# Optimization experiments

Measured on AMD Instinct MI355X. Metric: run time of the kernel, lower is better.

Reference implementation:

```python
import jax, jax.numpy as jnp
import numpy as np
from jax import lax

# Geometry derived from calc_block_params_and_padding_1d(32, 1024, 3, 1):
N, H, W, C = 1, 1024, 1024, 64
CO, K = 64, 3
BC = 32        # blocks per spatial dim (bcount)
BS = 34        # input block size (bsize)
BSO = 32       # output block size (bsize_out)
BSTR = 32      # block stride (bstride)
PAD = 1        # pad=2 total -> 1 top/left, 1 bottom/right
M = 512
EPS = 1e-3     # bn_eps


def setup_inputs() -> dict:
    key = jax.random.key(0)
    ks = jax.random.split(key, 8)
    inp_NHWC = jax.random.normal(ks[0], (N, H, W, C), jnp.float32)
    conv_w = jax.random.normal(ks[1], (K, K, C, CO), jnp.float32) * 0.05  # HWIO
    conv_b = jax.random.normal(ks[2], (CO,), jnp.float32) * 0.1
    gamma = 1.0 + 0.1 * jax.random.normal(ks[3], (CO,), jnp.float32)
    beta = 0.1 * jax.random.normal(ks[4], (CO,), jnp.float32)
    running_mean = 0.1 * jax.random.normal(ks[5], (CO,), jnp.float32)
    running_var = jax.random.uniform(ks[6], (CO,), jnp.float32, 0.5, 1.5)
    # active blocks: random subset of the 32x32 block grid, sorted flat ids
    flat = jnp.sort(jax.random.permutation(ks[7], BC * BC)[:M]).astype(jnp.int32)
    active_block_indices = jnp.stack(
        [jnp.zeros((M,), jnp.int32), flat // BC, flat % BC], axis=1)  # (n, i, j)
    return dict(inp_NHWC=inp_NHWC, conv_w=conv_w, conv_b=conv_b, gamma=gamma,
                beta=beta, running_mean=running_mean, running_var=running_var,
                active_block_indices=active_block_indices)


def reference(inp_NHWC, conv_w, conv_b, gamma, beta, running_mean, running_var,
              active_block_indices):
    # pad (as torch F.pad(0,0,1,1,1,1) on NHWC): pad H and W by 1 each side
    x = jnp.pad(inp_NHWC, ((0, 0), (PAD, PAD), (PAD, PAD), (0, 0)))
    n = active_block_indices[:, 0]
    i = active_block_indices[:, 1]
    j = active_block_indices[:, 2]

    # sparse_gather: extract [M, BS, BS, C] active tiles
    def gather(nn, ii, jj):
        return lax.dynamic_slice(x, (nn, ii * BSTR, jj * BSTR, 0), (1, BS, BS, C))[0]
    p = jax.vmap(gather)(n, i, j)  # [M, 34, 34, C]

    # conv (VALID, stride 1) + inference BatchNorm + ReLU
    q = lax.conv_general_dilated(p, conv_w, (1, 1), 'VALID',
                                 dimension_numbers=('NHWC', 'HWIO', 'NHWC'))
    q = q + conv_b
    scale = gamma * lax.rsqrt(running_var + EPS)
    q = jnp.maximum(q * scale + (beta - running_mean * scale), 0.0)  # [M, 32, 32, CO]

    # sparse_scatter (add=False): blocks tile the output exactly (BSO == BSTR)
    out6 = jnp.zeros((N, BC, BSO, BC, BSO, CO), inp_NHWC.dtype)
    out6 = out6.at[n, i, :, j].set(q)  # advanced idx -> [M, BSO, BSO, CO]
    return out6.reshape(N, BC * BSO, BC * BSO, CO)
```

## Files before the change

kernel.cpp:

```cpp
#include <hip/hip_runtime.h>

typedef _Float16 f16;
typedef f16 f16x8 __attribute__((ext_vector_type(8)));
typedef float f32x4 __attribute__((ext_vector_type(4)));

#define IMG_H 1024
#define IMG_W 1024
#define CIN 64
#define COUT_ 64
#define NBLK 32
#define NACT 512
#define EPS_ 1e-3f

#define WT_ELEMS (18 * 4 * 64 * 8)
#define WT_BYTES (WT_ELEMS * 2)
#define FLAGS_OFF WT_BYTES

__global__ void prep_weights_k(const float* __restrict__ w, f16* __restrict__ wt) {
    int t = blockIdx.x * 256 + threadIdx.x;
    if (t >= WT_ELEMS) return;
    int j  = t & 7;
    int l  = (t >> 3) & 63;
    int wv = (t >> 9) & 3;
    int kk = t >> 11;
    int ky = kk / 6;
    int kx = (kk % 6) >> 1;
    int hf = kk & 1;
    int cin  = hf * 32 + ((l >> 4) << 3) + j;
    int cout = wv * 16 + (l & 15);
    wt[t] = (f16)w[((ky * 3 + kx) * CIN + cin) * COUT_ + cout];
}

__global__ void prep_flags_k(const int* __restrict__ abi, int* __restrict__ flags) {
    int t = blockIdx.x * 256 + threadIdx.x;
    if (t < NACT) {
        int bi = abi[3 * t + 1];
        int bj = abi[3 * t + 2];
        flags[bi * NBLK + bj] = 1;
    }
}

__global__ void zero_inactive_k(const int* __restrict__ flags, float* __restrict__ out) {
    int b = blockIdx.x;
    if (flags[b]) return;
    int bi = b >> 5, bj = b & 31;
    float4 z = make_float4(0.f, 0.f, 0.f, 0.f);
    float4* base = (float4*)(out + ((size_t)(bi * 32) * IMG_W + bj * 32) * COUT_);
    for (int it = threadIdx.x; it < 32 * 512; it += 256) {
        int r  = it >> 9;
        int c4 = it & 511;
        base[(size_t)r * (IMG_W * COUT_ / 4) + c4] = z;
    }
}

__launch_bounds__(256, 2)
__global__ void sparse_conv_k(const float* __restrict__ inp,
                              const f16*  __restrict__ wt,
                              const float* __restrict__ cb,
                              const float* __restrict__ gamma,
                              const float* __restrict__ beta,
                              const float* __restrict__ rmean,
                              const float* __restrict__ rvar,
                              const int*  __restrict__ abi,
                              float* __restrict__ out) {
    __shared__ uint4 lds[18 * 34 * 8];

    const int wg = blockIdx.x;
    const int ab = wg >> 1, yh = wg & 1;
    const int bi = abi[3 * ab + 1];
    const int bj = abi[3 * ab + 2];
    const int tid  = threadIdx.x;
    const int lane = tid & 63;
    const int wv   = tid >> 6;

    const int r0 = bi * 32 + yh * 16 - 1;
    const int c0 = bj * 32 - 1;
    for (int task = tid; task < 18 * 34 * 8; task += 256) {
        int g  = task & 7;
        int p  = task >> 3;
        int dr = p / 34;
        int dc = p - dr * 34;
        int row = r0 + dr, col = c0 + dc;
        float4 a = make_float4(0.f, 0.f, 0.f, 0.f), b = a;
        if ((unsigned)row < IMG_H && (unsigned)col < IMG_W) {
            const float4* src = (const float4*)(inp + (((size_t)row * IMG_W + col) * CIN + g * 8));
            a = src[0]; b = src[1];
        }
        f16x8 v;
        v[0] = (f16)a.x; v[1] = (f16)a.y; v[2] = (f16)a.z; v[3] = (f16)a.w;
        v[4] = (f16)b.x; v[5] = (f16)b.y; v[6] = (f16)b.z; v[7] = (f16)b.w;
        lds[(p << 3) + (g ^ (dc & 7))] = __builtin_bit_cast(uint4, v);
    }

    f16x8 wf[18];
    const uint4* wt4 = (const uint4*)wt;
    #pragma unroll
    for (int kk = 0; kk < 18; ++kk)
        wf[kk] = __builtin_bit_cast(f16x8, wt4[(kk * 4 + wv) * 64 + lane]);

    const int co = wv * 16 + (lane & 15);
    const float sc = gamma[co] * rsqrtf(rvar[co] + EPS_);
    const float sh = cb[co] * sc + beta[co] - rmean[co] * sc;

    __syncthreads();

    const int pi   = lane & 15;
    const int kgrp = lane >> 4;
    float* outb = out + (((size_t)(bi * 32 + yh * 16) * IMG_W) + bj * 32) * COUT_;

    for (int yrow = 0; yrow < 16; ++yrow) {
        f32x4 acc0 = {0.f, 0.f, 0.f, 0.f};
        f32x4 acc1 = {0.f, 0.f, 0.f, 0.f};
        #pragma unroll
        for (int kk = 0; kk < 18; ++kk) {
            const int ky = kk / 6;
            const int kx = (kk % 6) >> 1;
            const int hf = kk & 1;
            const int dr = yrow + ky;
            const int g  = hf * 4 + kgrp;
            const int dc0 = pi + kx;
            const int dc1 = pi + kx + 16;
            uint4 a0 = lds[((dr * 34 + dc0) << 3) + (g ^ (dc0 & 7))];
            uint4 a1 = lds[((dr * 34 + dc1) << 3) + (g ^ (dc1 & 7))];
            acc0 = __builtin_amdgcn_mfma_f32_16x16x32_f16(__builtin_bit_cast(f16x8, a0), wf[kk], acc0, 0, 0, 0);
            acc1 = __builtin_amdgcn_mfma_f32_16x16x32_f16(__builtin_bit_cast(f16x8, a1), wf[kk], acc1, 0, 0, 0);
        }
        #pragma unroll
        for (int r = 0; r < 4; ++r) {
            const int px0 = kgrp * 4 + r;
            float v0 = fmaxf(acc0[r] * sc + sh, 0.f);
            float v1 = fmaxf(acc1[r] * sc + sh, 0.f);
            outb[((size_t)yrow * IMG_W + px0) * COUT_ + co] = v0;
            outb[((size_t)yrow * IMG_W + px0 + 16) * COUT_ + co] = v1;
        }
    }
}

extern "C" void kernel_launch(void* const* d_in, const int* in_sizes, int n_in,
                              void* d_out, int out_size, void* d_ws, size_t ws_size,
                              hipStream_t stream) {
    const float* inp   = (const float*)d_in[0];
    const float* convw = (const float*)d_in[1];
    const float* convb = (const float*)d_in[2];
    const float* gamma = (const float*)d_in[3];
    const float* beta  = (const float*)d_in[4];
    const float* rmean = (const float*)d_in[5];
    const float* rvar  = (const float*)d_in[6];
    const int*   abi   = (const int*)d_in[7];
    float* out = (float*)d_out;

    f16* wt    = (f16*)d_ws;
    int* flags = (int*)((char*)d_ws + FLAGS_OFF);

    hipMemsetAsync(flags, 0, NBLK * NBLK * sizeof(int), stream);
    hipLaunchKernelGGL(prep_flags_k, dim3(2), dim3(256), 0, stream, abi, flags);
    hipLaunchKernelGGL(prep_weights_k, dim3((WT_ELEMS + 255) / 256), dim3(256), 0, stream, convw, wt);
    hipLaunchKernelGGL(zero_inactive_k, dim3(NBLK * NBLK), dim3(256), 0, stream, flags, out);
    hipLaunchKernelGGL(sparse_conv_k, dim3(NACT * 2), dim3(256), 0, stream,
                       inp, wt, convb, gamma, beta, rmean, rvar, abi, out);
}
```

Measured before the change: 119.0 us.

## Fuse zero-fill into conv kernel and switch to 32x32x16 MFMA tiles

The flags memset, flag-prep kernel and zero-fill kernel are removed. Zeroing of inactive blocks now runs in extra workgroups of the conv kernel, each of which scans the active-index list in shared memory to decide whether its block is active. The conv inner loop moves from paired 16x16x32 MFMAs to 32x32x16 MFMAs with two alternating accumulators, and weights are re-laid out so each wave covers 32 output channels across 8 rows. This cuts launch overhead and changes the MFMA shape, but each wave now holds 36 weight fragments in registers, which may reduce occupancy.

```diff
diff --git a/kernel.cpp b/kernel.cpp
--- a/kernel.cpp
+++ b/kernel.cpp
@@ -2,7 +2,7 @@
 
 typedef _Float16 f16;
 typedef f16 f16x8 __attribute__((ext_vector_type(8)));
-typedef float f32x4 __attribute__((ext_vector_type(4)));
+typedef float f32x16 __attribute__((ext_vector_type(16)));
 
 #define IMG_H 1024
 #define IMG_W 1024
@@ -12,64 +12,61 @@
 #define NACT 512
 #define EPS_ 1e-3f
 
-#define WT_ELEMS (18 * 4 * 64 * 8)
-#define WT_BYTES (WT_ELEMS * 2)
-#define FLAGS_OFF WT_BYTES
+#define WT_ELEMS (36 * 2 * 64 * 8)
 
 __global__ void prep_weights_k(const float* __restrict__ w, f16* __restrict__ wt) {
     int t = blockIdx.x * 256 + threadIdx.x;
     if (t >= WT_ELEMS) return;
     int j  = t & 7;
     int l  = (t >> 3) & 63;
-    int wv = (t >> 9) & 3;
-    int kk = t >> 11;
-    int ky = kk / 6;
-    int kx = (kk % 6) >> 1;
-    int hf = kk & 1;
-    int cin  = hf * 32 + ((l >> 4) << 3) + j;
-    int cout = wv * 16 + (l & 15);
+    int ch = (t >> 9) & 1;
+    int ks = t >> 10;
+    int tap = ks >> 2, q = ks & 3;
+    int ky = tap / 3, kx = tap % 3;
+    int cin  = q * 16 + ((l >> 5) << 3) + j;
+    int cout = ch * 32 + (l & 31);
     wt[t] = (f16)w[((ky * 3 + kx) * CIN + cin) * COUT_ + cout];
 }
 
-__global__ void prep_flags_k(const int* __restrict__ abi, int* __restrict__ flags) {
-    int t = blockIdx.x * 256 + threadIdx.x;
-    if (t < NACT) {
-        int bi = abi[3 * t + 1];
-        int bj = abi[3 * t + 2];
-        flags[bi * NBLK + bj] = 1;
-    }
-}
-
-__global__ void zero_inactive_k(const int* __restrict__ flags, float* __restrict__ out) {
-    int b = blockIdx.x;
-    if (flags[b]) return;
-    int bi = b >> 5, bj = b & 31;
-    float4 z = make_float4(0.f, 0.f, 0.f, 0.f);
-    float4* base = (float4*)(out + ((size_t)(bi * 32) * IMG_W + bj * 32) * COUT_);
-    for (int it = threadIdx.x; it < 32 * 512; it += 256) {
-        int r  = it >> 9;
-        int c4 = it & 511;
-        base[(size_t)r * (IMG_W * COUT_ / 4) + c4] = z;
-    }
-}
-
 __launch_bounds__(256, 2)
-__global__ void sparse_conv_k(const float* __restrict__ inp,
-                              const f16*  __restrict__ wt,
-                              const float* __restrict__ cb,
-                              const float* __restrict__ gamma,
-                              const float* __restrict__ beta,
-                              const float* __restrict__ rmean,
-                              const float* __restrict__ rvar,
-                              const int*  __restrict__ abi,
-                              float* __restrict__ out) {
+__global__ void fused_k(const float* __restrict__ inp,
+                        const f16*  __restrict__ wt,
+                        const float* __restrict__ cb,
+                        const float* __restrict__ gamma,
+                        const float* __restrict__ beta,
+                        const float* __restrict__ rmean,
+                        const float* __restrict__ rvar,
+                        const int*  __restrict__ abi,
+                        float* __restrict__ out) {
     __shared__ uint4 lds[18 * 34 * 8];
+    __shared__ int act;
 
     const int wg = blockIdx.x;
+    const int tid = threadIdx.x;
+
+    if (wg >= 2 * NACT) {
+        int b  = wg - 2 * NACT;
+        int bi = b >> 5, bj = b & 31;
+        if (tid == 0) act = 0;
+        __syncthreads();
+        int e0 = 2 * tid, e1 = 2 * tid + 1;
+        if (abi[3 * e0 + 1] == bi && abi[3 * e0 + 2] == bj) act = 1;
+        if (abi[3 * e1 + 1] == bi && abi[3 * e1 + 2] == bj) act = 1;
+        __syncthreads();
+        if (act) return;
+        float4 z = make_float4(0.f, 0.f, 0.f, 0.f);
+        float4* base = (float4*)(out + ((size_t)(bi * 32) * IMG_W + bj * 32) * COUT_);
+        for (int it = tid; it < 32 * 512; it += 256) {
+            int r  = it >> 9;
+            int c4 = it & 511;
+            base[(size_t)r * (IMG_W * COUT_ / 4) + c4] = z;
+        }
+        return;
+    }
+
     const int ab = wg >> 1, yh = wg & 1;
     const int bi = abi[3 * ab + 1];
     const int bj = abi[3 * ab + 2];
-    const int tid  = threadIdx.x;
     const int lane = tid & 63;
     const int wv   = tid >> 6;
 
@@ -92,46 +89,46 @@
         lds[(p << 3) + (g ^ (dc & 7))] = __builtin_bit_cast(uint4, v);
     }
 
-    f16x8 wf[18];
+    const int rg  = wv & 1;
+    const int chh = wv >> 1;
+    f16x8 wf[36];
     const uint4* wt4 = (const uint4*)wt;
     #pragma unroll
-    for (int kk = 0; kk < 18; ++kk)
-        wf[kk] = __builtin_bit_cast(f16x8, wt4[(kk * 4 + wv) * 64 + lane]);
+    for (int ks = 0; ks < 36; ++ks)
+        wf[ks] = __builtin_bit_cast(f16x8, wt4[(ks * 2 + chh) * 64 + lane]);
 
-    const int co = wv * 16 + (lane & 15);
+    const int co = chh * 32 + (lane & 31);
     const float sc = gamma[co] * rsqrtf(rvar[co] + EPS_);
     const float sh = cb[co] * sc + beta[co] - rmean[co] * sc;
 
     __syncthreads();
 
-    const int pi   = lane & 15;
-    const int kgrp = lane >> 4;
+    const int px = lane & 31;
+    const int hi = lane >> 5;
     float* outb = out + (((size_t)(bi * 32 + yh * 16) * IMG_W) + bj * 32) * COUT_;
 
-    for (int yrow = 0; yrow < 16; ++yrow) {
-        f32x4 acc0 = {0.f, 0.f, 0.f, 0.f};
-        f32x4 acc1 = {0.f, 0.f, 0.f, 0.f};
+    for (int yr = 0; yr < 8; ++yr) {
+        const int R = rg * 8 + yr;
+        f32x16 accA = {0.f,0.f,0.f,0.f,0.f,0.f,0.f,0.f,0.f,0.f,0.f,0.f,0.f,0.f,0.f,0.f};
+        f32x16 accB = {0.f,0.f,0.f,0.f,0.f,0.f,0.f,0.f,0.f,0.f,0.f,0.f,0.f,0.f,0.f,0.f};
         #pragma unroll
-        for (int kk = 0; kk < 18; ++kk) {
-            const int ky = kk / 6;
-            const int kx = (kk % 6) >> 1;
-            const int hf = kk & 1;
-            const int dr = yrow + ky;
-            const int g  = hf * 4 + kgrp;
-            const int dc0 = pi + kx;
-            const int dc1 = pi + kx + 16;
-            uint4 a0 = lds[((dr * 34 + dc0) << 3) + (g ^ (dc0 & 7))];
-            uint4 a1 = lds[((dr * 34 + dc1) << 3) + (g ^ (dc1 & 7))];
-            acc0 = __builtin_amdgcn_mfma_f32_16x16x32_f16(__builtin_bit_cast(f16x8, a0), wf[kk], acc0, 0, 0, 0);
-            acc1 = __builtin_amdgcn_mfma_f32_16x16x32_f16(__builtin_bit_cast(f16x8, a1), wf[kk], acc1, 0, 0, 0);
+        for (int ks = 0; ks < 36; ++ks) {
+            const int tap = ks >> 2, q = ks & 3;
+            const int ky = tap / 3, kx = tap % 3;
+            const int dr = R + ky;
+            const int dc = px + kx;
+            const int slot = (q * 2 + hi) ^ (dc & 7);
+            uint4 a = lds[((dr * 34 + dc) << 3) + slot];
+            if (ks & 1)
+                accB = __builtin_amdgcn_mfma_f32_32x32x16_f16(__builtin_bit_cast(f16x8, a), wf[ks], accB, 0, 0, 0);
+            else
+                accA = __builtin_amdgcn_mfma_f32_32x32x16_f16(__builtin_bit_cast(f16x8, a), wf[ks], accA, 0, 0, 0);
         }
         #pragma unroll
-        for (int r = 0; r < 4; ++r) {
-            const int px0 = kgrp * 4 + r;
-            float v0 = fmaxf(acc0[r] * sc + sh, 0.f);
-            float v1 = fmaxf(acc1[r] * sc + sh, 0.f);
-            outb[((size_t)yrow * IMG_W + px0) * COUT_ + co] = v0;
-            outb[((size_t)yrow * IMG_W + px0 + 16) * COUT_ + co] = v1;
+        for (int r = 0; r < 16; ++r) {
+            const int pxo = (r & 3) + 8 * (r >> 2) + 4 * hi;
+            float v = fmaxf((accA[r] + accB[r]) * sc + sh, 0.f);
+            outb[((size_t)R * IMG_W + pxo) * COUT_ + co] = v;
         }
     }
 }
@@ -149,13 +146,9 @@
     const int*   abi   = (const int*)d_in[7];
     float* out = (float*)d_out;
 
-    f16* wt    = (f16*)d_ws;
-    int* flags = (int*)((char*)d_ws + FLAGS_OFF);
+    f16* wt = (f16*)d_ws;
 
-    hipMemsetAsync(flags, 0, NBLK * NBLK * sizeof(int), stream);
-    hipLaunchKernelGGL(prep_flags_k, dim3(2), dim3(256), 0, stream, abi, flags);
     hipLaunchKernelGGL(prep_weights_k, dim3((WT_ELEMS + 255) / 256), dim3(256), 0, stream, convw, wt);
-    hipLaunchKernelGGL(zero_inactive_k, dim3(NBLK * NBLK), dim3(256), 0, stream, flags, out);
-    hipLaunchKernelGGL(sparse_conv_k, dim3(NACT * 2), dim3(256), 0, stream,
+    hipLaunchKernelGGL(fused_k, dim3(2 * NACT + NBLK * NBLK), dim3(256), 0, stream,
                        inp, wt, convb, gamma, beta, rmean, rvar, abi, out);
 }
```

Result: faster. 108.8 us (-8.5%).
